# Performance work log

Measured on AMD Instinct MI355X. Metric: run time of the kernel, lower is better.

Reference implementation:

```python
import jax, jax.numpy as jnp
import numpy as np

B, H, S, D = 4, 16, 2048, 64

def setup_inputs() -> dict:
    key = jax.random.key(0)
    kq, kk, kv = jax.random.split(key, 3)
    return {
        "input_query": jax.random.normal(kq, (B, H, S, D), dtype=jnp.float32),
        "input_key": jax.random.normal(kk, (B, H, S, D), dtype=jnp.float32),
        "input_value": jax.random.normal(kv, (B, H, S, D), dtype=jnp.float32),
    }

def reference(input_query, input_key, input_value):
    # Unscaled, unmasked attention: softmax(Q K^T) V
    scores = jnp.einsum("bhsd,bhtd->bhst", input_query, input_key)  # [B,H,S,S]
    probs = jax.nn.softmax(scores, axis=-1)
    return jnp.einsum("bhst,bhtd->bhsd", probs, input_value)  # [B,H,S,D]
```

## Files before the change

### kernel.cpp

```cpp
#include <hip/hip_runtime.h>
#include <hip/hip_bf16.h>
#include <stdint.h>

#define SEQ 2048
#define DIM 64
#define NH  64
#define KT  32
#define TILE_BYTES 12288
#define KF_BYTES   8192

typedef __attribute__((ext_vector_type(8)))  short    bf16x8;
typedef __attribute__((ext_vector_type(8)))  _Float16 f16x8;
typedef __attribute__((ext_vector_type(16))) float    f32x16;
typedef unsigned int u32;

#if __has_builtin(__builtin_amdgcn_exp2f)
#define EXP2(x) __builtin_amdgcn_exp2f(x)
#else
#define EXP2(x) exp2f(x)
#endif

__device__ __forceinline__ int phi(int s) {
    int h = (s >> 2) & 1, b = s >> 3, i = s & 3;
    return 8 * h + 4 * b + i + (b >= 2 ? 8 : 0);
}
__device__ __forceinline__ short f2bf(float f) {
    union { float f; u32 u; } v; v.f = f;
    u32 r = v.u + 0x7fffu + ((v.u >> 16) & 1u);
    return (short)(r >> 16);
}

__global__ __launch_bounds__(256) void prep(const float* __restrict__ K,
                                            const float* __restrict__ V,
                                            char* __restrict__ ws) {
    __shared__ float Ks[KT][68];
    __shared__ float Vs[KT][68];
    const int blk = blockIdx.x;
    const size_t src = (size_t)blk * (KT * DIM);
    const int t = threadIdx.x;
    #pragma unroll
    for (int i = 0; i < 2; ++i) {
        int e = (t + i * 256) * 4;
        int r = e >> 6, c = e & 63;
        *(float4*)&Ks[r][c] = *(const float4*)(K + src + e);
        *(float4*)&Vs[r][c] = *(const float4*)(V + src + e);
    }
    __syncthreads();
    char* blob = ws + (size_t)blk * TILE_BYTES;
    {
        const int c = t >> 6, lane = t & 63, col = lane & 31, h = lane >> 5;
        const int row = phi(col), d0 = c * 16 + 8 * h;
        f16x8 hi, lo;
        #pragma unroll
        for (int j = 0; j < 8; ++j) {
            float x = Ks[row][d0 + j];
            _Float16 xh = (_Float16)x;
            hi[j] = xh;
            lo[j] = (_Float16)(x - (float)xh);
        }
        *(f16x8*)(blob + (c * 2 + 0) * 1024 + lane * 16) = hi;
        *(f16x8*)(blob + (c * 2 + 1) * 1024 + lane * 16) = lo;
    }
    {
        const int f = t >> 7, c = (t >> 6) & 1, lane = t & 63, col = lane & 31, h = lane >> 5;
        bf16x8 v;
        #pragma unroll
        for (int j = 0; j < 8; ++j) {
            int key = phi(16 * c + 8 * h + j);
            v[j] = f2bf(Vs[key][f * 32 + col]);
        }
        *(bf16x8*)(blob + KF_BYTES + (f * 2 + c) * 1024 + lane * 16) = v;
    }
}

__device__ __forceinline__ void stage(const char* g, char* l, int wave, int lane) {
    #pragma unroll
    for (int i = 0; i < 3; ++i) {
        const char* gp = g + i * 4096 + wave * 1024 + lane * 16;
        char* lp = l + i * 4096 + wave * 1024;
        __builtin_amdgcn_global_load_lds(
            (const __attribute__((address_space(1))) u32*)gp,
            (__attribute__((address_space(3))) u32*)lp, 16, 0, 0);
    }
}

__global__ __launch_bounds__(256, 2) void attn_fwd(
    const float* __restrict__ Q, const char* __restrict__ ws,
    float* __restrict__ O)
{
    __shared__ __align__(16) char buf[2][TILE_BYTES];

    const int tid  = threadIdx.x;
    const int wave = tid >> 6, lane = tid & 63;
    const int h = lane >> 5, col = lane & 31;
    const int head = blockIdx.x >> 3;
    const int qb = (blockIdx.x & 7) * 256 + wave * 64;
    const size_t base = (size_t)head * SEQ * DIM;

    f16x8 qf[2][4];
    #pragma unroll
    for (int qt = 0; qt < 2; ++qt) {
        const float* qr = Q + base + (size_t)(qb + qt * 32 + col) * DIM;
        #pragma unroll
        for (int c = 0; c < 4; ++c)
            #pragma unroll
            for (int j = 0; j < 8; ++j)
                qf[qt][c][j] = (_Float16)(qr[c * 16 + 8 * h + j] * 1.44269504088896f);
    }

    f32x16 z16;
    #pragma unroll
    for (int r = 0; r < 16; ++r) z16[r] = 0.f;
    f32x16 of[2][2];
    of[0][0] = z16; of[0][1] = z16; of[1][0] = z16; of[1][1] = z16;
    float l_own[2] = {0.f, 0.f};

    const char* blob0 = ws + (size_t)head * 64 * TILE_BYTES;
    stage(blob0, buf[0], wave, lane);

    for (int kt = 0; kt < SEQ / KT; ++kt) {
        __syncthreads();
        if (kt + 1 < SEQ / KT)
            stage(blob0 + (size_t)(kt + 1) * TILE_BYTES, buf[(kt + 1) & 1], wave, lane);
        const char* cur = buf[kt & 1];

        f32x16 s[2]; s[0] = z16; s[1] = z16;
        #pragma unroll
        for (int c = 0; c < 4; ++c) {
            f16x8 kh = *(const f16x8*)(cur + (c * 2 + 0) * 1024 + lane * 16);
            f16x8 kl = *(const f16x8*)(cur + (c * 2 + 1) * 1024 + lane * 16);
            s[0] = __builtin_amdgcn_mfma_f32_32x32x16_f16(kh, qf[0][c], s[0], 0, 0, 0);
            s[0] = __builtin_amdgcn_mfma_f32_32x32x16_f16(kl, qf[0][c], s[0], 0, 0, 0);
            s[1] = __builtin_amdgcn_mfma_f32_32x32x16_f16(kh, qf[1][c], s[1], 0, 0, 0);
            s[1] = __builtin_amdgcn_mfma_f32_32x32x16_f16(kl, qf[1][c], s[1], 0, 0, 0);
        }

        bf16x8 pfrag[2][2];
        #pragma unroll
        for (int qt = 0; qt < 2; ++qt) {
            float p[16], ls = 0.f;
            #pragma unroll
            for (int r = 0; r < 16; ++r) { p[r] = EXP2(s[qt][r]); ls += p[r]; }
            l_own[qt] += ls;
            u32 pk[8], sw[8];
            #pragma unroll
            for (int m = 0; m < 8; ++m) {
                __hip_bfloat162 b2 = __float22bfloat162_rn(make_float2(p[2 * m], p[2 * m + 1]));
                __builtin_memcpy(&pk[m], &b2, 4);
            }
            #pragma unroll
            for (int m = 0; m < 8; ++m) sw[m] = __shfl_xor(pk[m], 32);
            #pragma unroll
            for (int c = 0; c < 2; ++c) {
                union { u32 w[4]; bf16x8 v; } fr;
                fr.w[0] = h ? sw[4 * c + 2] : pk[4 * c + 0];
                fr.w[1] = h ? sw[4 * c + 3] : pk[4 * c + 1];
                fr.w[2] = h ? pk[4 * c + 2] : sw[4 * c + 0];
                fr.w[3] = h ? pk[4 * c + 3] : sw[4 * c + 1];
                pfrag[qt][c] = fr.v;
            }
        }

        #pragma unroll
        for (int f = 0; f < 2; ++f)
            #pragma unroll
            for (int c = 0; c < 2; ++c) {
                bf16x8 vf = *(const bf16x8*)(cur + KF_BYTES + (f * 2 + c) * 1024 + lane * 16);
                of[0][f] = __builtin_amdgcn_mfma_f32_32x32x16_bf16(pfrag[0][c], vf, of[0][f], 0, 0, 0);
                of[1][f] = __builtin_amdgcn_mfma_f32_32x32x16_bf16(pfrag[1][c], vf, of[1][f], 0, 0, 0);
            }
    }

    float* op = O + base;
    #pragma unroll
    for (int qt = 0; qt < 2; ++qt) {
        float lall = l_own[qt] + __shfl_xor(l_own[qt], 32);
        float inv = 1.0f / lall;
        #pragma unroll
        for (int r = 0; r < 16; ++r) {
            int qrow = (r & 3) + 8 * (r >> 2) + 4 * h;
            float iq = __shfl(inv, qrow);
            op[(size_t)(qb + qt * 32 + qrow) * DIM + col]      = of[qt][0][r] * iq;
            op[(size_t)(qb + qt * 32 + qrow) * DIM + 32 + col] = of[qt][1][r] * iq;
        }
    }
}

extern "C" void kernel_launch(void* const* d_in, const int* in_sizes, int n_in,
                              void* d_out, int out_size, void* d_ws, size_t ws_size,
                              hipStream_t stream) {
    const float* Q = (const float*)d_in[0];
    const float* K = (const float*)d_in[1];
    const float* V = (const float*)d_in[2];
    float* Out = (float*)d_out;
    char* ws = (char*)d_ws;

    prep<<<dim3(NH * (SEQ / KT)), dim3(256), 0, stream>>>(K, V, ws);
    attn_fwd<<<dim3(NH * (SEQ / 256)), dim3(256), 0, stream>>>(Q, ws, Out);
}
```

Measured before the change: 247.5 us.

## Fuse K/V preprocessing into attention kernel with in-loop tile conversion

Removes the separate prep kernel and its workspace round trip. Each attention block now streams raw fp32 K/V tiles into LDS with async global-to-LDS loads, using an XOR swizzle on K. It converts them in-loop to fp16 hi/lo and bf16 MFMA fragments, with a two-deep raw and fragment pipeline. The trade-off is that every query block of a head redoes the conversion, adding VALU and LDS work to the main loop and roughly doubling LDS use per block.

```diff
diff --git a/kernel.cpp b/kernel.cpp
--- a/kernel.cpp
+++ b/kernel.cpp
@@ -6,7 +6,9 @@
 #define DIM 64
 #define NH  64
 #define KT  32
-#define TILE_BYTES 12288
+#define NT  (SEQ / KT)
+#define RAW_BYTES  16384
+#define FRAG_BYTES 12288
 #define KF_BYTES   8192
 
 typedef __attribute__((ext_vector_type(8)))  short    bf16x8;
@@ -30,65 +32,62 @@
     return (short)(r >> 16);
 }
 
-__global__ __launch_bounds__(256) void prep(const float* __restrict__ K,
-                                            const float* __restrict__ V,
-                                            char* __restrict__ ws) {
-    __shared__ float Ks[KT][68];
-    __shared__ float Vs[KT][68];
-    const int blk = blockIdx.x;
-    const size_t src = (size_t)blk * (KT * DIM);
-    const int t = threadIdx.x;
+__device__ __forceinline__ void stage_tile(const float* gK, const float* gV,
+                                           char* raw, int wave, int lane) {
     #pragma unroll
     for (int i = 0; i < 2; ++i) {
-        int e = (t + i * 256) * 4;
-        int r = e >> 6, c = e & 63;
-        *(float4*)&Ks[r][c] = *(const float4*)(K + src + e);
-        *(float4*)&Vs[r][c] = *(const float4*)(V + src + e);
-    }
-    __syncthreads();
-    char* blob = ws + (size_t)blk * TILE_BYTES;
+        const int P  = wave * 128 + i * 64 + lane;
+        const int sk = (P & ~15) | ((P & 15) ^ ((P >> 4) & 7));
+        char* dK = raw + (size_t)(wave * 128 + i * 64) * 16;
+        char* dV = raw + 8192 + (size_t)(wave * 128 + i * 64) * 16;
+        __builtin_amdgcn_global_load_lds(
+            (const __attribute__((address_space(1))) u32*)((const char*)gK + (size_t)sk * 16),
+            (__attribute__((address_space(3))) u32*)dK, 16, 0, 0);
+        __builtin_amdgcn_global_load_lds(
+            (const __attribute__((address_space(1))) u32*)((const char*)gV + (size_t)P * 16),
+            (__attribute__((address_space(3))) u32*)dV, 16, 0, 0);
+    }
+}
+
+__device__ __forceinline__ void convert_tile(const char* raw, char* frag, int t) {
+    const int lane = t & 63, col = lane & 31, h = lane >> 5;
     {
-        const int c = t >> 6, lane = t & 63, col = lane & 31, h = lane >> 5;
-        const int row = phi(col), d0 = c * 16 + 8 * h;
+        const int c = t >> 6;
+        const int r = phi(col);
+        const int kk = 4 * c + 2 * h;
+        const float4* rk = (const float4*)raw;
+        float4 a = rk[r * 16 + ((kk    ) ^ (r & 7))];
+        float4 b = rk[r * 16 + ((kk + 1) ^ (r & 7))];
+        float x[8] = {a.x, a.y, a.z, a.w, b.x, b.y, b.z, b.w};
         f16x8 hi, lo;
         #pragma unroll
         for (int j = 0; j < 8; ++j) {
-            float x = Ks[row][d0 + j];
-            _Float16 xh = (_Float16)x;
+            _Float16 xh = (_Float16)x[j];
             hi[j] = xh;
-            lo[j] = (_Float16)(x - (float)xh);
-        }
-        *(f16x8*)(blob + (c * 2 + 0) * 1024 + lane * 16) = hi;
-        *(f16x8*)(blob + (c * 2 + 1) * 1024 + lane * 16) = lo;
+            lo[j] = (_Float16)(x[j] - (float)xh);
+        }
+        *(f16x8*)(frag + (c * 2 + 0) * 1024 + lane * 16) = hi;
+        *(f16x8*)(frag + (c * 2 + 1) * 1024 + lane * 16) = lo;
     }
     {
-        const int f = t >> 7, c = (t >> 6) & 1, lane = t & 63, col = lane & 31, h = lane >> 5;
+        const int f = t >> 7, c = (t >> 6) & 1;
+        const float* rv = (const float*)(raw + 8192);
         bf16x8 v;
         #pragma unroll
         for (int j = 0; j < 8; ++j) {
             int key = phi(16 * c + 8 * h + j);
-            v[j] = f2bf(Vs[key][f * 32 + col]);
-        }
-        *(bf16x8*)(blob + KF_BYTES + (f * 2 + c) * 1024 + lane * 16) = v;
-    }
-}
-
-__device__ __forceinline__ void stage(const char* g, char* l, int wave, int lane) {
-    #pragma unroll
-    for (int i = 0; i < 3; ++i) {
-        const char* gp = g + i * 4096 + wave * 1024 + lane * 16;
-        char* lp = l + i * 4096 + wave * 1024;
-        __builtin_amdgcn_global_load_lds(
-            (const __attribute__((address_space(1))) u32*)gp,
-            (__attribute__((address_space(3))) u32*)lp, 16, 0, 0);
-    }
-}
-
-__global__ __launch_bounds__(256, 2) void attn_fwd(
-    const float* __restrict__ Q, const char* __restrict__ ws,
-    float* __restrict__ O)
+            v[j] = f2bf(rv[key * 64 + f * 32 + col]);
+        }
+        *(bf16x8*)(frag + KF_BYTES + (f * 2 + c) * 1024 + lane * 16) = v;
+    }
+}
+
+__global__ __launch_bounds__(256, 2) void attn_fused(
+    const float* __restrict__ Q, const float* __restrict__ K,
+    const float* __restrict__ V, float* __restrict__ O)
 {
-    __shared__ __align__(16) char buf[2][TILE_BYTES];
+    __shared__ __align__(16) char raw[2][RAW_BYTES];
+    __shared__ __align__(16) char frag[2][FRAG_BYTES];
 
     const int tid  = threadIdx.x;
     const int wave = tid >> 6, lane = tid & 63;
@@ -96,6 +95,8 @@
     const int head = blockIdx.x >> 3;
     const int qb = (blockIdx.x & 7) * 256 + wave * 64;
     const size_t base = (size_t)head * SEQ * DIM;
+    const float* Kh = K + base;
+    const float* Vh = V + base;
 
     f16x8 qf[2][4];
     #pragma unroll
@@ -115,14 +116,17 @@
     of[0][0] = z16; of[0][1] = z16; of[1][0] = z16; of[1][1] = z16;
     float l_own[2] = {0.f, 0.f};
 
-    const char* blob0 = ws + (size_t)head * 64 * TILE_BYTES;
-    stage(blob0, buf[0], wave, lane);
-
-    for (int kt = 0; kt < SEQ / KT; ++kt) {
+    stage_tile(Kh, Vh, raw[0], wave, lane);
+    __syncthreads();
+    convert_tile(raw[0], frag[0], tid);
+    stage_tile(Kh + KT * DIM, Vh + KT * DIM, raw[1], wave, lane);
+
+    for (int kt = 0; kt < NT; ++kt) {
         __syncthreads();
-        if (kt + 1 < SEQ / KT)
-            stage(blob0 + (size_t)(kt + 1) * TILE_BYTES, buf[(kt + 1) & 1], wave, lane);
-        const char* cur = buf[kt & 1];
+        if (kt < NT - 2)
+            stage_tile(Kh + (size_t)(kt + 2) * KT * DIM,
+                       Vh + (size_t)(kt + 2) * KT * DIM, raw[kt & 1], wave, lane);
+        const char* cur = frag[kt & 1];
 
         f32x16 s[2]; s[0] = z16; s[1] = z16;
         #pragma unroll
@@ -169,6 +173,9 @@
                 of[0][f] = __builtin_amdgcn_mfma_f32_32x32x16_bf16(pfrag[0][c], vf, of[0][f], 0, 0, 0);
                 of[1][f] = __builtin_amdgcn_mfma_f32_32x32x16_bf16(pfrag[1][c], vf, of[1][f], 0, 0, 0);
             }
+
+        if (kt < NT - 1)
+            convert_tile(raw[(kt + 1) & 1], frag[(kt + 1) & 1], tid);
     }
 
     float* op = O + base;
@@ -193,8 +200,7 @@
     const float* K = (const float*)d_in[1];
     const float* V = (const float*)d_in[2];
     float* Out = (float*)d_out;
-    char* ws = (char*)d_ws;
-
-    prep<<<dim3(NH * (SEQ / KT)), dim3(256), 0, stream>>>(K, V, ws);
-    attn_fwd<<<dim3(NH * (SEQ / 256)), dim3(256), 0, stream>>>(Q, ws, Out);
-}
+    (void)d_ws; (void)ws_size;
+
+    attn_fused<<<dim3(NH * (SEQ / 256)), dim3(256), 0, stream>>>(Q, K, V, Out);
+}
```

Measured after the change: 238.5 us. -3.6%, faster.
